# Performance work log

Hardware: AMD Instinct MI355X
Metric: run time of the kernel (lower is better)

The kernel has to match this reference:

```python
import jax, jax.numpy as jnp
import numpy as np

EPS = 1e-7

# Poincare ball, curvature c = 1 (hyparticle-net default manifold)

def _mobius_add(x, y):
    x2 = jnp.sum(x * x, axis=-1, keepdims=True)
    y2 = jnp.sum(y * y, axis=-1, keepdims=True)
    xy = jnp.sum(x * y, axis=-1, keepdims=True)
    num = (1.0 + 2.0 * xy + y2) * x + (1.0 - x2) * y
    den = 1.0 + 2.0 * xy + x2 * y2
    return num / jnp.maximum(den, EPS)


def _lambda_x(x):
    # conformal factor lambda_x = 2 / (1 - ||x||^2)
    return 2.0 / jnp.clip(1.0 - jnp.sum(x * x, axis=-1, keepdims=True), EPS, None)


def _logmap(y, x):
    # log map of y at base point x
    u = _mobius_add(-x, y)
    un = jnp.clip(jnp.linalg.norm(u, axis=-1, keepdims=True), EPS, 1.0 - 1e-5)
    return (2.0 / _lambda_x(x)) * jnp.arctanh(un) * (u / un)


def _expmap(v, x):
    # exp map of tangent vector v at base point x
    vn = jnp.clip(jnp.linalg.norm(v, axis=-1, keepdims=True), EPS, None)
    second = jnp.tanh(_lambda_x(x) * vn * 0.5) * (v / vn)
    return _mobius_add(x, second)


def setup_inputs() -> dict:
    key = jax.random.key(0)
    k1, k2 = jax.random.split(key)
    N, D = 1024, 64
    u = jax.random.normal(k1, (N, D), dtype=jnp.float32)
    # points strictly inside the unit ball (norm < 0.5)
    x = 0.5 * u / (1.0 + jnp.linalg.norm(u, axis=-1, keepdims=True))
    adj = jax.random.randint(k2, (N, N), 0, 2, dtype=jnp.int32)
    return {"x": x, "adj": adj}


def reference(x, adj):
    mask = adj > 0                                   # [N, N]
    # all-pairs logmap: logs[i, j] = log_{x_i}(x_j)   [N, N, D]
    logs = jax.vmap(lambda xi: _logmap(x, xi))(x)
    v = jnp.sum(jnp.where(mask[..., None], logs, 0.0), axis=1)  # [N, D]
    return _expmap(v, x)                             # [N, D]
```

## Files before the change

### kernel.cpp

```cpp
#include <hip/hip_runtime.h>

#define EPSF 1e-7f

__device__ __forceinline__ float rcp_fast(float x) { return __builtin_amdgcn_rcpf(x); }

__device__ __forceinline__ int swz(int r, int c) { return r * 16 + (c ^ ((r >> 2) & 7)); }

__device__ __forceinline__ float dot4(float4 v) {
    return v.x * v.x + v.y * v.y + v.z * v.z + v.w * v.w;
}

__global__ __launch_bounds__(256, 2) void pair_kernel(
    const float* __restrict__ x, const int* __restrict__ adj,
    float* __restrict__ T, float* __restrict__ alphaPart) {
    const int N = 1024;
    const int j0 = blockIdx.x * 64;
    const int i0 = blockIdx.y * 32;
    const int t = threadIdx.x;
    const int h = t & 1;
    const int q = t >> 1;
    const int qx = q & 15;
    const int qy = q >> 4;

    __shared__ float4 ti4[32 * 16];
    __shared__ float4 tj4[64 * 16];
    __shared__ float x2i_l[32];
    __shared__ float y2_l[64];

    const float4* x4 = reinterpret_cast<const float4*>(x);
#pragma unroll
    for (int k = 0; k < 2; ++k) {
        const int f = k * 256 + t;
        const int r = f >> 4, c = f & 15;
        float4 v = x4[(size_t)i0 * 16 + f];
        ti4[swz(r, c)] = v;
        float s = dot4(v);
#pragma unroll
        for (int off = 1; off <= 8; off <<= 1) s += __shfl_xor(s, off, 64);
        if ((t & 15) == 0) x2i_l[r] = s;
    }
#pragma unroll
    for (int k = 0; k < 4; ++k) {
        const int f = k * 256 + t;
        const int r = f >> 4, c = f & 15;
        float4 v = x4[(size_t)j0 * 16 + f];
        tj4[swz(r, c)] = v;
        float s = dot4(v);
#pragma unroll
        for (int off = 1; off <= 8; off <<= 1) s += __shfl_xor(s, off, 64);
        if ((t & 15) == 0) y2_l[r] = s;
    }
    __syncthreads();

    float acc[4][4];
#pragma unroll
    for (int a = 0; a < 4; ++a)
#pragma unroll
        for (int b = 0; b < 4; ++b) acc[a][b] = 0.f;

#pragma unroll
    for (int cc = 0; cc < 8; ++cc) {
        const int c = h * 8 + cc;
        float4 xiv[4], xjv[4];
#pragma unroll
        for (int a = 0; a < 4; ++a) xiv[a] = ti4[swz(qy * 4 + a, c)];
#pragma unroll
        for (int b = 0; b < 4; ++b) xjv[b] = tj4[swz(qx * 4 + b, c)];
#pragma unroll
        for (int a = 0; a < 4; ++a)
#pragma unroll
            for (int b = 0; b < 4; ++b) {
                acc[a][b] = fmaf(xiv[a].x, xjv[b].x, acc[a][b]);
                acc[a][b] = fmaf(xiv[a].y, xjv[b].y, acc[a][b]);
                acc[a][b] = fmaf(xiv[a].z, xjv[b].z, acc[a][b]);
                acc[a][b] = fmaf(xiv[a].w, xjv[b].w, acc[a][b]);
            }
    }
#pragma unroll
    for (int a = 0; a < 4; ++a)
#pragma unroll
        for (int b = 0; b < 4; ++b) acc[a][b] += __shfl_xor(acc[a][b], 1, 64);

    const int ib = i0 + qy * 4;
    const int jb = j0 + qx * 4;
    const int bsel = h * 2;
    const float y2[2] = {y2_l[qx * 4 + bsel], y2_l[qx * 4 + bsel + 1]};

    float svsum[4];
#pragma unroll
    for (int a = 0; a < 4; ++a) {
        const int2 aj = *reinterpret_cast<const int2*>(&adj[(size_t)(ib + a) * N + jb + bsel]);
        const int m[2] = {aj.x, aj.y};
        const float x2a = x2i_l[qy * 4 + a];
        const float onemx2 = 1.f - x2a;
        const float onemx2c = fmaxf(onemx2, EPSF);
        float tv2[2];
        float ssum = 0.f;
#pragma unroll
        for (int bb = 0; bb < 2; ++bb) {
            const float dot = acc[a][bsel + bb];
            const float c1 = fmaf(-2.f, dot, 1.f);
            const float A = c1 + y2[bb];
            const float den = fmaxf(fmaf(x2a, y2[bb], c1), EPSF);
            const float rd = rcp_fast(den);
            const float av = -A * rd;
            const float bv = onemx2 * rd;
            float un2 = av * av * x2a;
            un2 = fmaf(bv * bv, y2[bb], un2);
            un2 = fmaf(2.f * av * bv, dot, un2);
            un2 = fmaxf(un2, 0.f);
            float un = sqrtf(un2);
            un = fminf(fmaxf(un, EPSF), 1.0f - 1e-5f);
            const float ratio = (1.f + un) * rcp_fast(1.f - un);
            const float at = 0.34657359027997264f * __log2f(ratio);
            const float g = onemx2c * at * rcp_fast(un);
            const float sv = m[bb] ? g * av : 0.f;
            const float tv = m[bb] ? g * bv : 0.f;
            ssum += sv;
            tv2[bb] = tv;
        }
        float2 tw = {tv2[0], tv2[1]};
        *reinterpret_cast<float2*>(&T[(size_t)(ib + a) * N + jb + bsel]) = tw;
        svsum[a] = ssum;
    }

#pragma unroll
    for (int off = 1; off <= 16; off <<= 1) {
#pragma unroll
        for (int a = 0; a < 4; ++a) svsum[a] += __shfl_xor(svsum[a], off, 64);
    }
    if ((t & 31) == 0) {
#pragma unroll
        for (int a = 0; a < 4; ++a)
            alphaPart[(size_t)blockIdx.x * N + ib + a] = svsum[a];
    }
}

__global__ __launch_bounds__(256, 2) void out_kernel(
    const float* __restrict__ x, const float* __restrict__ T,
    const float* __restrict__ alphaPart, float* __restrict__ out) {
    const int N = 1024, D = 64;
    const int i0 = blockIdx.x * 2;
    const int w = threadIdx.x >> 6;
    const int d = threadIdx.x & 63;
    const int jw = __builtin_amdgcn_readfirstlane(w * 256);

    const float4* T0 = reinterpret_cast<const float4*>(T + (size_t)i0 * N + jw);
    const float4* T1 = reinterpret_cast<const float4*>(T + (size_t)(i0 + 1) * N + jw);
    const float* xbase = x + (size_t)jw * D + d;

    float a0 = 0.f, a1 = 0.f, a2 = 0.f, a3 = 0.f;
    float b0 = 0.f, b1 = 0.f, b2 = 0.f, b3 = 0.f;
#pragma unroll 4
    for (int qq = 0; qq < 64; ++qq) {
        const float4 t0 = T0[qq];
        const float4 t1 = T1[qq];
        const float* xp = xbase + (size_t)qq * 4 * D;
        const float x0 = xp[0 * D], x1 = xp[1 * D], x2v = xp[2 * D], x3 = xp[3 * D];
        a0 = fmaf(t0.x, x0, a0);  b0 = fmaf(t1.x, x0, b0);
        a1 = fmaf(t0.y, x1, a1);  b1 = fmaf(t1.y, x1, b1);
        a2 = fmaf(t0.z, x2v, a2); b2 = fmaf(t1.z, x2v, b2);
        a3 = fmaf(t0.w, x3, a3);  b3 = fmaf(t1.w, x3, b3);
    }

    __shared__ float part[2][4][64];
    part[0][w][d] = (a0 + a1) + (a2 + a3);
    part[1][w][d] = (b0 + b1) + (b2 + b3);
    __syncthreads();

    if (threadIdx.x < 128) {
        const int r = threadIdx.x >> 6;
        const int i = i0 + r;
        float v = (part[r][0][d] + part[r][1][d]) + (part[r][2][d] + part[r][3][d]);

        float ap = (d < 16) ? alphaPart[(size_t)d * N + i] : 0.f;
#pragma unroll
        for (int off = 1; off < 64; off <<= 1) ap += __shfl_xor(ap, off, 64);

        const float xid = x[(size_t)i * D + d];
        float x2i = xid * xid;
#pragma unroll
        for (int off = 1; off < 64; off <<= 1) x2i += __shfl_xor(x2i, off, 64);
        const float onemx2 = 1.f - x2i;
        const float onemx2c = fmaxf(onemx2, EPSF);
        v = fmaf(ap, xid, v);

        float vn2 = v * v;
#pragma unroll
        for (int off = 1; off < 64; off <<= 1) vn2 += __shfl_xor(vn2, off, 64);
        const float vn = fmaxf(sqrtf(vn2), EPSF);
        const float arg = vn * rcp_fast(onemx2c);
        const float th = tanhf(arg);
        const float sec = th * rcp_fast(vn) * v;

        float xy = xid * sec;
        float y2p = sec * sec;
#pragma unroll
        for (int off = 1; off < 64; off <<= 1) {
            xy += __shfl_xor(xy, off, 64);
            y2p += __shfl_xor(y2p, off, 64);
        }
        const float numd = (1.f + 2.f * xy + y2p) * xid + onemx2 * sec;
        const float den2 = fmaxf(fmaf(x2i, y2p, 1.f + 2.f * xy), EPSF);
        out[(size_t)i * D + d] = numd * rcp_fast(den2);
    }
}

extern "C" void kernel_launch(void* const* d_in, const int* in_sizes, int n_in,
                              void* d_out, int out_size, void* d_ws, size_t ws_size,
                              hipStream_t stream) {
    const float* x = (const float*)d_in[0];
    const int* adj = (const int*)d_in[1];
    float* out = (float*)d_out;
    const int N = 1024;

    float* T = (float*)d_ws;
    float* alphaPart = (float*)((char*)d_ws + (size_t)N * N * 4);

    hipLaunchKernelGGL(pair_kernel, dim3(16, 32), dim3(256), 0, stream, x, adj, T, alphaPart);
    hipLaunchKernelGGL(out_kernel, dim3(N / 2), dim3(256), 0, stream, x, T, alphaPart, out);
}
```

Before: 23.52 us.

## Fuse pair and output kernels into one cooperative launch with grid sync

Merges the pairwise logmap kernel and the aggregation/expmap kernel into a single cooperative kernel of 512 blocks, with a grid-wide barrier between the two phases. Shared memory from the first phase is reused for the partial sums of the second. The aim is to remove the second kernel launch and the gap between kernels. The cost is a grid sync, and all 512 blocks must be co-resident, which the launch-bounds hint of 2 blocks per CU should allow on a 256-CU part. Cooperative launch may carry its own overhead.

```diff
diff --git a/kernel.cpp b/kernel.cpp
--- a/kernel.cpp
+++ b/kernel.cpp
@@ -1,4 +1,7 @@
 #include <hip/hip_runtime.h>
+#include <hip/hip_cooperative_groups.h>
+
+namespace cg = cooperative_groups;
 
 #define EPSF 1e-7f
 
@@ -10,199 +13,203 @@
     return v.x * v.x + v.y * v.y + v.z * v.z + v.w * v.w;
 }
 
-__global__ __launch_bounds__(256, 2) void pair_kernel(
+__global__ __launch_bounds__(256, 2) void fused_kernel(
     const float* __restrict__ x, const int* __restrict__ adj,
-    float* __restrict__ T, float* __restrict__ alphaPart) {
-    const int N = 1024;
-    const int j0 = blockIdx.x * 64;
-    const int i0 = blockIdx.y * 32;
+    float* __restrict__ T, float* __restrict__ alphaPart,
+    float* __restrict__ out) {
+    const int N = 1024, D = 64;
     const int t = threadIdx.x;
-    const int h = t & 1;
-    const int q = t >> 1;
-    const int qx = q & 15;
-    const int qy = q >> 4;
 
     __shared__ float4 ti4[32 * 16];
     __shared__ float4 tj4[64 * 16];
     __shared__ float x2i_l[32];
     __shared__ float y2_l[64];
 
-    const float4* x4 = reinterpret_cast<const float4*>(x);
-#pragma unroll
-    for (int k = 0; k < 2; ++k) {
-        const int f = k * 256 + t;
-        const int r = f >> 4, c = f & 15;
-        float4 v = x4[(size_t)i0 * 16 + f];
-        ti4[swz(r, c)] = v;
-        float s = dot4(v);
-#pragma unroll
-        for (int off = 1; off <= 8; off <<= 1) s += __shfl_xor(s, off, 64);
-        if ((t & 15) == 0) x2i_l[r] = s;
+    {
+        const int jt = blockIdx.x & 15;
+        const int j0 = jt * 64;
+        const int i0 = (blockIdx.x >> 4) * 32;
+        const int h = t & 1;
+        const int q = t >> 1;
+        const int qx = q & 15;
+        const int qy = q >> 4;
+
+        const float4* x4 = reinterpret_cast<const float4*>(x);
+#pragma unroll
+        for (int k = 0; k < 2; ++k) {
+            const int f = k * 256 + t;
+            const int r = f >> 4, c = f & 15;
+            float4 v = x4[(size_t)i0 * 16 + f];
+            ti4[swz(r, c)] = v;
+            float s = dot4(v);
+#pragma unroll
+            for (int off = 1; off <= 8; off <<= 1) s += __shfl_xor(s, off, 64);
+            if ((t & 15) == 0) x2i_l[r] = s;
+        }
+#pragma unroll
+        for (int k = 0; k < 4; ++k) {
+            const int f = k * 256 + t;
+            const int r = f >> 4, c = f & 15;
+            float4 v = x4[(size_t)j0 * 16 + f];
+            tj4[swz(r, c)] = v;
+            float s = dot4(v);
+#pragma unroll
+            for (int off = 1; off <= 8; off <<= 1) s += __shfl_xor(s, off, 64);
+            if ((t & 15) == 0) y2_l[r] = s;
+        }
+        __syncthreads();
+
+        float acc[4][4];
+#pragma unroll
+        for (int a = 0; a < 4; ++a)
+#pragma unroll
+            for (int b = 0; b < 4; ++b) acc[a][b] = 0.f;
+
+#pragma unroll
+        for (int cc = 0; cc < 8; ++cc) {
+            const int c = h * 8 + cc;
+            float4 xiv[4], xjv[4];
+#pragma unroll
+            for (int a = 0; a < 4; ++a) xiv[a] = ti4[swz(qy * 4 + a, c)];
+#pragma unroll
+            for (int b = 0; b < 4; ++b) xjv[b] = tj4[swz(qx * 4 + b, c)];
+#pragma unroll
+            for (int a = 0; a < 4; ++a)
+#pragma unroll
+                for (int b = 0; b < 4; ++b) {
+                    acc[a][b] = fmaf(xiv[a].x, xjv[b].x, acc[a][b]);
+                    acc[a][b] = fmaf(xiv[a].y, xjv[b].y, acc[a][b]);
+                    acc[a][b] = fmaf(xiv[a].z, xjv[b].z, acc[a][b]);
+                    acc[a][b] = fmaf(xiv[a].w, xjv[b].w, acc[a][b]);
+                }
+        }
+#pragma unroll
+        for (int a = 0; a < 4; ++a)
+#pragma unroll
+            for (int b = 0; b < 4; ++b) acc[a][b] += __shfl_xor(acc[a][b], 1, 64);
+
+        const int ib = i0 + qy * 4;
+        const int jb = j0 + qx * 4;
+        const int bsel = h * 2;
+        const float y2[2] = {y2_l[qx * 4 + bsel], y2_l[qx * 4 + bsel + 1]};
+
+        float svsum[4];
+#pragma unroll
+        for (int a = 0; a < 4; ++a) {
+            const int2 aj = *reinterpret_cast<const int2*>(&adj[(size_t)(ib + a) * N + jb + bsel]);
+            const int m[2] = {aj.x, aj.y};
+            const float x2a = x2i_l[qy * 4 + a];
+            const float onemx2 = 1.f - x2a;
+            const float onemx2c = fmaxf(onemx2, EPSF);
+            float tv2[2];
+            float ssum = 0.f;
+#pragma unroll
+            for (int bb = 0; bb < 2; ++bb) {
+                const float dot = acc[a][bsel + bb];
+                const float c1 = fmaf(-2.f, dot, 1.f);
+                const float A = c1 + y2[bb];
+                const float den = fmaxf(fmaf(x2a, y2[bb], c1), EPSF);
+                const float rd = rcp_fast(den);
+                const float av = -A * rd;
+                const float bv = onemx2 * rd;
+                float un2 = av * av * x2a;
+                un2 = fmaf(bv * bv, y2[bb], un2);
+                un2 = fmaf(2.f * av * bv, dot, un2);
+                un2 = fmaxf(un2, 0.f);
+                float un = sqrtf(un2);
+                un = fminf(fmaxf(un, EPSF), 1.0f - 1e-5f);
+                const float ratio = (1.f + un) * rcp_fast(1.f - un);
+                const float at = 0.34657359027997264f * __log2f(ratio);
+                const float g = onemx2c * at * rcp_fast(un);
+                const float sv = m[bb] ? g * av : 0.f;
+                const float tv = m[bb] ? g * bv : 0.f;
+                ssum += sv;
+                tv2[bb] = tv;
+            }
+            float2 tw = {tv2[0], tv2[1]};
+            *reinterpret_cast<float2*>(&T[(size_t)(ib + a) * N + jb + bsel]) = tw;
+            svsum[a] = ssum;
+        }
+
+#pragma unroll
+        for (int off = 1; off <= 16; off <<= 1) {
+#pragma unroll
+            for (int a = 0; a < 4; ++a) svsum[a] += __shfl_xor(svsum[a], off, 64);
+        }
+        if ((t & 31) == 0) {
+#pragma unroll
+            for (int a = 0; a < 4; ++a)
+                alphaPart[(size_t)jt * N + ib + a] = svsum[a];
+        }
     }
-#pragma unroll
-    for (int k = 0; k < 4; ++k) {
-        const int f = k * 256 + t;
-        const int r = f >> 4, c = f & 15;
-        float4 v = x4[(size_t)j0 * 16 + f];
-        tj4[swz(r, c)] = v;
-        float s = dot4(v);
-#pragma unroll
-        for (int off = 1; off <= 8; off <<= 1) s += __shfl_xor(s, off, 64);
-        if ((t & 15) == 0) y2_l[r] = s;
-    }
-    __syncthreads();
-
-    float acc[4][4];
-#pragma unroll
-    for (int a = 0; a < 4; ++a)
-#pragma unroll
-        for (int b = 0; b < 4; ++b) acc[a][b] = 0.f;
-
-#pragma unroll
-    for (int cc = 0; cc < 8; ++cc) {
-        const int c = h * 8 + cc;
-        float4 xiv[4], xjv[4];
-#pragma unroll
-        for (int a = 0; a < 4; ++a) xiv[a] = ti4[swz(qy * 4 + a, c)];
-#pragma unroll
-        for (int b = 0; b < 4; ++b) xjv[b] = tj4[swz(qx * 4 + b, c)];
-#pragma unroll
-        for (int a = 0; a < 4; ++a)
-#pragma unroll
-            for (int b = 0; b < 4; ++b) {
-                acc[a][b] = fmaf(xiv[a].x, xjv[b].x, acc[a][b]);
-                acc[a][b] = fmaf(xiv[a].y, xjv[b].y, acc[a][b]);
-                acc[a][b] = fmaf(xiv[a].z, xjv[b].z, acc[a][b]);
-                acc[a][b] = fmaf(xiv[a].w, xjv[b].w, acc[a][b]);
+
+    cg::this_grid().sync();
+
+    {
+        const int i0 = blockIdx.x * 2;
+        const int w = t >> 6;
+        const int d = t & 63;
+        const int jw = __builtin_amdgcn_readfirstlane(w * 256);
+
+        const float4* T0 = reinterpret_cast<const float4*>(T + (size_t)i0 * N + jw);
+        const float4* T1 = reinterpret_cast<const float4*>(T + (size_t)(i0 + 1) * N + jw);
+        const float* xbase = x + (size_t)jw * D + d;
+
+        float a0 = 0.f, a1 = 0.f, a2 = 0.f, a3 = 0.f;
+        float b0 = 0.f, b1 = 0.f, b2 = 0.f, b3 = 0.f;
+#pragma unroll 4
+        for (int qq = 0; qq < 64; ++qq) {
+            const float4 t0 = T0[qq];
+            const float4 t1 = T1[qq];
+            const float* xp = xbase + (size_t)qq * 4 * D;
+            const float x0 = xp[0 * D], x1 = xp[1 * D], x2v = xp[2 * D], x3 = xp[3 * D];
+            a0 = fmaf(t0.x, x0, a0);  b0 = fmaf(t1.x, x0, b0);
+            a1 = fmaf(t0.y, x1, a1);  b1 = fmaf(t1.y, x1, b1);
+            a2 = fmaf(t0.z, x2v, a2); b2 = fmaf(t1.z, x2v, b2);
+            a3 = fmaf(t0.w, x3, a3);  b3 = fmaf(t1.w, x3, b3);
+        }
+
+        float (*part)[4][64] = reinterpret_cast<float (*)[4][64]>(ti4);
+        part[0][w][d] = (a0 + a1) + (a2 + a3);
+        part[1][w][d] = (b0 + b1) + (b2 + b3);
+        __syncthreads();
+
+        if (t < 128) {
+            const int r = t >> 6;
+            const int i = i0 + r;
+            float v = (part[r][0][d] + part[r][1][d]) + (part[r][2][d] + part[r][3][d]);
+
+            float ap = (d < 16) ? alphaPart[(size_t)d * N + i] : 0.f;
+#pragma unroll
+            for (int off = 1; off < 64; off <<= 1) ap += __shfl_xor(ap, off, 64);
+
+            const float xid = x[(size_t)i * D + d];
+            float x2i = xid * xid;
+#pragma unroll
+            for (int off = 1; off < 64; off <<= 1) x2i += __shfl_xor(x2i, off, 64);
+            const float onemx2 = 1.f - x2i;
+            const float onemx2c = fmaxf(onemx2, EPSF);
+            v = fmaf(ap, xid, v);
+
+            float vn2 = v * v;
+#pragma unroll
+            for (int off = 1; off < 64; off <<= 1) vn2 += __shfl_xor(vn2, off, 64);
+            const float vn = fmaxf(sqrtf(vn2), EPSF);
+            const float arg = vn * rcp_fast(onemx2c);
+            const float th = tanhf(arg);
+            const float sec = th * rcp_fast(vn) * v;
+
+            float xy = xid * sec;
+            float y2p = sec * sec;
+#pragma unroll
+            for (int off = 1; off < 64; off <<= 1) {
+                xy += __shfl_xor(xy, off, 64);
+                y2p += __shfl_xor(y2p, off, 64);
             }
-    }
-#pragma unroll
-    for (int a = 0; a < 4; ++a)
-#pragma unroll
-        for (int b = 0; b < 4; ++b) acc[a][b] += __shfl_xor(acc[a][b], 1, 64);
-
-    const int ib = i0 + qy * 4;
-    const int jb = j0 + qx * 4;
-    const int bsel = h * 2;
-    const float y2[2] = {y2_l[qx * 4 + bsel], y2_l[qx * 4 + bsel + 1]};
-
-    float svsum[4];
-#pragma unroll
-    for (int a = 0; a < 4; ++a) {
-        const int2 aj = *reinterpret_cast<const int2*>(&adj[(size_t)(ib + a) * N + jb + bsel]);
-        const int m[2] = {aj.x, aj.y};
-        const float x2a = x2i_l[qy * 4 + a];
-        const float onemx2 = 1.f - x2a;
-        const float onemx2c = fmaxf(onemx2, EPSF);
-        float tv2[2];
-        float ssum = 0.f;
-#pragma unroll
-        for (int bb = 0; bb < 2; ++bb) {
-            const float dot = acc[a][bsel + bb];
-            const float c1 = fmaf(-2.f, dot, 1.f);
-            const float A = c1 + y2[bb];
-            const float den = fmaxf(fmaf(x2a, y2[bb], c1), EPSF);
-            const float rd = rcp_fast(den);
-            const float av = -A * rd;
-            const float bv = onemx2 * rd;
-            float un2 = av * av * x2a;
-            un2 = fmaf(bv * bv, y2[bb], un2);
-            un2 = fmaf(2.f * av * bv, dot, un2);
-            un2 = fmaxf(un2, 0.f);
-            float un = sqrtf(un2);
-            un = fminf(fmaxf(un, EPSF), 1.0f - 1e-5f);
-            const float ratio = (1.f + un) * rcp_fast(1.f - un);
-            const float at = 0.34657359027997264f * __log2f(ratio);
-            const float g = onemx2c * at * rcp_fast(un);
-            const float sv = m[bb] ? g * av : 0.f;
-            const float tv = m[bb] ? g * bv : 0.f;
-            ssum += sv;
-            tv2[bb] = tv;
-        }
-        float2 tw = {tv2[0], tv2[1]};
-        *reinterpret_cast<float2*>(&T[(size_t)(ib + a) * N + jb + bsel]) = tw;
-        svsum[a] = ssum;
-    }
-
-#pragma unroll
-    for (int off = 1; off <= 16; off <<= 1) {
-#pragma unroll
-        for (int a = 0; a < 4; ++a) svsum[a] += __shfl_xor(svsum[a], off, 64);
-    }
-    if ((t & 31) == 0) {
-#pragma unroll
-        for (int a = 0; a < 4; ++a)
-            alphaPart[(size_t)blockIdx.x * N + ib + a] = svsum[a];
-    }
-}
-
-__global__ __launch_bounds__(256, 2) void out_kernel(
-    const float* __restrict__ x, const float* __restrict__ T,
-    const float* __restrict__ alphaPart, float* __restrict__ out) {
-    const int N = 1024, D = 64;
-    const int i0 = blockIdx.x * 2;
-    const int w = threadIdx.x >> 6;
-    const int d = threadIdx.x & 63;
-    const int jw = __builtin_amdgcn_readfirstlane(w * 256);
-
-    const float4* T0 = reinterpret_cast<const float4*>(T + (size_t)i0 * N + jw);
-    const float4* T1 = reinterpret_cast<const float4*>(T + (size_t)(i0 + 1) * N + jw);
-    const float* xbase = x + (size_t)jw * D + d;
-
-    float a0 = 0.f, a1 = 0.f, a2 = 0.f, a3 = 0.f;
-    float b0 = 0.f, b1 = 0.f, b2 = 0.f, b3 = 0.f;
-#pragma unroll 4
-    for (int qq = 0; qq < 64; ++qq) {
-        const float4 t0 = T0[qq];
-        const float4 t1 = T1[qq];
-        const float* xp = xbase + (size_t)qq * 4 * D;
-        const float x0 = xp[0 * D], x1 = xp[1 * D], x2v = xp[2 * D], x3 = xp[3 * D];
-        a0 = fmaf(t0.x, x0, a0);  b0 = fmaf(t1.x, x0, b0);
-        a1 = fmaf(t0.y, x1, a1);  b1 = fmaf(t1.y, x1, b1);
-        a2 = fmaf(t0.z, x2v, a2); b2 = fmaf(t1.z, x2v, b2);
-        a3 = fmaf(t0.w, x3, a3);  b3 = fmaf(t1.w, x3, b3);
-    }
-
-    __shared__ float part[2][4][64];
-    part[0][w][d] = (a0 + a1) + (a2 + a3);
-    part[1][w][d] = (b0 + b1) + (b2 + b3);
-    __syncthreads();
-
-    if (threadIdx.x < 128) {
-        const int r = threadIdx.x >> 6;
-        const int i = i0 + r;
-        float v = (part[r][0][d] + part[r][1][d]) + (part[r][2][d] + part[r][3][d]);
-
-        float ap = (d < 16) ? alphaPart[(size_t)d * N + i] : 0.f;
-#pragma unroll
-        for (int off = 1; off < 64; off <<= 1) ap += __shfl_xor(ap, off, 64);
-
-        const float xid = x[(size_t)i * D + d];
-        float x2i = xid * xid;
-#pragma unroll
-        for (int off = 1; off < 64; off <<= 1) x2i += __shfl_xor(x2i, off, 64);
-        const float onemx2 = 1.f - x2i;
-        const float onemx2c = fmaxf(onemx2, EPSF);
-        v = fmaf(ap, xid, v);
-
-        float vn2 = v * v;
-#pragma unroll
-        for (int off = 1; off < 64; off <<= 1) vn2 += __shfl_xor(vn2, off, 64);
-        const float vn = fmaxf(sqrtf(vn2), EPSF);
-        const float arg = vn * rcp_fast(onemx2c);
-        const float th = tanhf(arg);
-        const float sec = th * rcp_fast(vn) * v;
-
-        float xy = xid * sec;
-        float y2p = sec * sec;
-#pragma unroll
-        for (int off = 1; off < 64; off <<= 1) {
-            xy += __shfl_xor(xy, off, 64);
-            y2p += __shfl_xor(y2p, off, 64);
-        }
-        const float numd = (1.f + 2.f * xy + y2p) * xid + onemx2 * sec;
-        const float den2 = fmaxf(fmaf(x2i, y2p, 1.f + 2.f * xy), EPSF);
-        out[(size_t)i * D + d] = numd * rcp_fast(den2);
+            const float numd = (1.f + 2.f * xy + y2p) * xid + onemx2 * sec;
+            const float den2 = fmaxf(fmaf(x2i, y2p, 1.f + 2.f * xy), EPSF);
+            out[(size_t)i * D + d] = numd * rcp_fast(den2);
+        }
     }
 }
 
@@ -217,6 +224,7 @@
     float* T = (float*)d_ws;
     float* alphaPart = (float*)((char*)d_ws + (size_t)N * N * 4);
 
-    hipLaunchKernelGGL(pair_kernel, dim3(16, 32), dim3(256), 0, stream, x, adj, T, alphaPart);
-    hipLaunchKernelGGL(out_kernel, dim3(N / 2), dim3(256), 0, stream, x, T, alphaPart, out);
+    void* args[] = {(void*)&x, (void*)&adj, (void*)&T, (void*)&alphaPart, (void*)&out};
+    hipLaunchCooperativeKernel((const void*)fused_kernel, dim3(512), dim3(256),
+                               args, 0, stream);
 }
```

Measured after the change: 91.06 us. 287% more time.
